# Kernel optimization log

Measured on AMD Instinct MI355X. Metric: run time of the kernel, lower is better.

Reference implementation:

```python
import jax, jax.numpy as jnp
import numpy as np

L_POS, L_DIR, H = 10, 4, 128
N = 1048576

def posenc(x, L):
    feats = [x]
    for j in range(L):
        s = (2.0 ** j) * x
        feats.append(jnp.sin(s))
        feats.append(jnp.cos(s))
    return jnp.concatenate(feats, axis=1)

def _w(key, fan_in, fan_out):
    return jax.random.normal(key, (fan_in, fan_out), dtype=jnp.float32) * (1.0 / np.sqrt(fan_in))

def setup_inputs() -> dict:
    key = jax.random.key(0)
    ks = jax.random.split(key, 16)
    pos = jax.random.normal(ks[0], (N, 3), dtype=jnp.float32)
    dirs = jax.random.normal(ks[1], (N, 3), dtype=jnp.float32)
    d_pos = 3 + 2 * 3 * L_POS  # 63
    d_dir = 3 + 2 * 3 * L_DIR  # 27
    inp = {
        'pos': pos, 'dirs': dirs,
        # block1: 4 hidden layers, ReLU everywhere incl. output (bias-free tcnn MLP)
        'b1_w0': _w(ks[2], d_pos, H), 'b1_w1': _w(ks[3], H, H),
        'b1_w2': _w(ks[4], H, H),    'b1_w3': _w(ks[5], H, H),
        'b1_w4': _w(ks[6], H, H),
        # block2: 3 hidden layers, linear output of width H+1
        'b2_w0': _w(ks[7], H + d_pos, H), 'b2_w1': _w(ks[8], H, H),
        'b2_w2': _w(ks[9], H, H),         'b2_w3': _w(ks[10], H, H + 1),
        # block3: 1 hidden layer of H//2, sigmoid output of width 3
        'b3_w0': _w(ks[11], H + d_dir, H // 2), 'b3_w1': _w(ks[12], H // 2, 3),
    }
    return inp

def reference(pos, dirs, b1_w0, b1_w1, b1_w2, b1_w3, b1_w4,
              b2_w0, b2_w1, b2_w2, b2_w3, b3_w0, b3_w1):
    relu = jax.nn.relu
    x_emb = posenc(pos, L_POS)   # [N, 63]
    d_emb = posenc(dirs, L_DIR)  # [N, 27]
    # block1: ReLU hidden + ReLU output
    h = relu(x_emb @ b1_w0)
    h = relu(h @ b1_w1)
    h = relu(h @ b1_w2)
    h = relu(h @ b1_w3)
    h = relu(h @ b1_w4)          # [N, 128]
    # block2: ReLU hidden, linear output
    g = relu(jnp.concatenate([h, x_emb], axis=1) @ b2_w0)
    g = relu(g @ b2_w1)
    g = relu(g @ b2_w2)
    g = g @ b2_w3                # [N, 129]
    sigma = jax.nn.relu(g[:, -1])
    feat = g[:, :-1]             # [N, 128]
    # block3: ReLU hidden, sigmoid output
    c = relu(jnp.concatenate([feat, d_emb], axis=1) @ b3_w0)
    color = jax.nn.sigmoid(c @ b3_w1)  # [N, 3]
    return (color, sigma)
```

## Files before the change

### kernel.cpp

```cpp
#include <hip/hip_runtime.h>
#include <hip/hip_bf16.h>

#define NTOT  1048576
#define MWG   128
#define BLK   256
#define ROWB  400
#define ACT_BYTES  (MWG * ROWB)

typedef __attribute__((ext_vector_type(8))) short  bf16x8;
typedef __attribute__((ext_vector_type(4))) float  f32x4;

__device__ __forceinline__ unsigned short f2bf(float f) {
  unsigned u = __float_as_uint(f);
  u += 0x7fffu + ((u >> 16) & 1u);
  return (unsigned short)(u >> 16);
}

__device__ __forceinline__ unsigned pk2bf(float lo, float hi) {
  float2 t; t.x = lo; t.y = hi;
  __hip_bfloat162 b = __float22bfloat162_rn(t);
  return *(unsigned*)&b;
}

__global__ __launch_bounds__(256) void prepack_k(
    const float* __restrict__ s0, const float* __restrict__ s1,
    const float* __restrict__ s2, const float* __restrict__ s3,
    const float* __restrict__ s4, const float* __restrict__ s5,
    const float* __restrict__ s6, const float* __restrict__ s7,
    const float* __restrict__ s8, const float* __restrict__ s9,
    const float* __restrict__ s10, unsigned short* __restrict__ dst)
{
  const int nw_[11]  = {128,128,128,128,128,128,128,128,144, 64, 16};
  const int kw_[11]  = { 64,128,128,128,128,192,128,128,128,192, 64};
  const int nc_[11]  = {128,128,128,128,128,128,128,128,129, 64,  3};
  const int k1_[11]  = { 63,128,128,128,128, 63,128,128,128, 27, 64};
  const int o1_[11]  = {  0,  0,  0,  0,  0,128,  0,  0,  0,128,  0};
  const int k2_[11]  = {999,999,999,999,999, 64,999,999,999, 64,999};
  const int do_[11]  = {0,8192,24576,40960,57344,73728,98304,114688,131072,149504,161792};

  int c = blockIdx.x;
  const float* src =
    c==0?s0: c==1?s1: c==2?s2: c==3?s3: c==4?s4: c==5?s5:
    c==6?s6: c==7?s7: c==8?s8: c==9?s9: s10;
  int nw=nw_[c], kw=kw_[c], nc=nc_[c], k1=k1_[c], o1=o1_[c], k2=k2_[c];
  int KS = kw >> 5;
  int total = nw * kw;
  for (int idx = blockIdx.y * blockDim.x + threadIdx.x; idx < total;
       idx += gridDim.y * blockDim.x) {
    int e   = idx & 7;
    int l15 = (idx >> 3) & 15;
    int lg  = (idx >> 7) & 3;
    int r   = idx >> 9;
    int ks  = r % KS;
    int nt  = r / KS;
    int n = nt * 16 + l15;
    int k = ks * 32 + lg * 8 + e;
    float v = 0.f;
    if (n < nc) {
      if (k < k1)       v = src[(o1 + k) * nc + n];
      else if (k >= k2) v = src[(k - k2) * nc + n];
    }
    dst[do_[c] + idx] = f2bf(v);
  }
}

template<int I0, int L>
__device__ __forceinline__ void posenc_store(unsigned char* actb, int row,
                                             float p0, float p1, float p2)
{
#pragma unroll
  for (int q = 0; q < 4; q++) {
    float hv[8];
#pragma unroll
    for (int e = 0; e < 8; e++) {
      const int i = I0 + q * 8 + e;
      float v;
      if (i == 0) v = p0;
      else if (i == 1) v = p1;
      else if (i == 2) v = p2;
      else {
        const int idx = i - 3, j = idx / 6, t = idx % 6;
        if (j < L) {
          const float sc = (float)(1 << j);
          const float a  = (t % 3 == 0 ? p0 : (t % 3 == 1 ? p1 : p2)) * sc;
          v = (t < 3) ? __sinf(a) : __cosf(a);
        } else v = 0.f;
      }
      hv[e] = v;
    }
    uint4 pk;
    pk.x = pk2bf(hv[0], hv[1]);
    pk.y = pk2bf(hv[2], hv[3]);
    pk.z = pk2bf(hv[4], hv[5]);
    pk.w = pk2bf(hv[6], hv[7]);
    *(uint4*)(actb + row * ROWB + (I0 + q * 8) * 2) = pk;
  }
}

template<int KS, int KB, int DST, bool RELU, bool MIDBAR, bool SIG>
__device__ __forceinline__ void layer22(
    unsigned char* actb, const unsigned short* __restrict__ wchunk,
    const unsigned* rbase, const unsigned* wbase,
    int lane, int wid, float* __restrict__ out, long grow0)
{
  const int l15 = lane & 15;
  const int lg  = lane >> 4;
  const int wn  = wid & 1;
  const unsigned short* wl = wchunk + (wn * 4) * (KS * 512) + lane * 8;
  const f32x4 vzero = {0.f, 0.f, 0.f, 0.f};
  f32x4 acc[4][4];

  {
    bf16x8 afr[4];
#pragma unroll
    for (int nt = 0; nt < 4; nt++)
      afr[nt] = *(const bf16x8*)(wl + (nt * KS) * 512);
    bf16x8 bfr4[4];
#pragma unroll
    for (int mq = 0; mq < 4; mq++)
      bfr4[mq] = *(const bf16x8*)(actb + rbase[mq] + KB * 2);
#pragma unroll
    for (int nt = 0; nt < 4; nt++)
#pragma unroll
      for (int mq = 0; mq < 4; mq++)
        acc[mq][nt] = __builtin_amdgcn_mfma_f32_16x16x32_bf16(
            afr[nt], bfr4[mq], vzero, 0, 0, 0);
  }
#pragma unroll
  for (int ks = 1; ks < KS; ks++) {
    bf16x8 afr[4];
#pragma unroll
    for (int nt = 0; nt < 4; nt++)
      afr[nt] = *(const bf16x8*)(wl + (nt * KS + ks) * 512);
    bf16x8 bfr4[4];
#pragma unroll
    for (int mq = 0; mq < 4; mq++)
      bfr4[mq] = *(const bf16x8*)(actb + rbase[mq] + (KB * 2 + ks * 64));
#pragma unroll
    for (int nt = 0; nt < 4; nt++)
#pragma unroll
      for (int mq = 0; mq < 4; mq++)
        acc[mq][nt] = __builtin_amdgcn_mfma_f32_16x16x32_bf16(
            afr[nt], bfr4[mq], acc[mq][nt], 0, 0, 0);
  }

  f32x4 accs[2];
  if (SIG) {
    unsigned sbase0 = ((2 * wid + 0) * 16 + l15) * ROWB + lg * 16;
    unsigned sbase1 = ((2 * wid + 1) * 16 + l15) * ROWB + lg * 16;
    {
      bf16x8 afs = *(const bf16x8*)(wchunk + (8 * KS) * 512 + lane * 8);
      bf16x8 b0 = *(const bf16x8*)(actb + sbase0 + KB * 2);
      bf16x8 b1 = *(const bf16x8*)(actb + sbase1 + KB * 2);
      accs[0] = __builtin_amdgcn_mfma_f32_16x16x32_bf16(afs, b0, vzero, 0, 0, 0);
      accs[1] = __builtin_amdgcn_mfma_f32_16x16x32_bf16(afs, b1, vzero, 0, 0, 0);
    }
#pragma unroll
    for (int ks = 1; ks < KS; ks++) {
      bf16x8 afs = *(const bf16x8*)(wchunk + (8 * KS + ks) * 512 + lane * 8);
      bf16x8 b0 = *(const bf16x8*)(actb + sbase0 + (KB * 2 + ks * 64));
      bf16x8 b1 = *(const bf16x8*)(actb + sbase1 + (KB * 2 + ks * 64));
      accs[0] = __builtin_amdgcn_mfma_f32_16x16x32_bf16(afs, b0, accs[0], 0, 0, 0);
      accs[1] = __builtin_amdgcn_mfma_f32_16x16x32_bf16(afs, b1, accs[1], 0, 0, 0);
    }
  }

  if (MIDBAR) __syncthreads();

#pragma unroll
  for (int mq = 0; mq < 4; mq++) {
#pragma unroll
    for (int nt = 0; nt < 4; nt++) {
      f32x4 v = acc[mq][nt];
      if (RELU) {
        v.x = fmaxf(v.x, 0.f); v.y = fmaxf(v.y, 0.f);
        v.z = fmaxf(v.z, 0.f); v.w = fmaxf(v.w, 0.f);
      }
      uint2 pk;
      pk.x = pk2bf(v.x, v.y);
      pk.y = pk2bf(v.z, v.w);
      *(uint2*)(actb + wbase[mq] + (DST * 2 + nt * 32)) = pk;
    }
  }
  if (SIG && lg == 0) {
#pragma unroll
    for (int j = 0; j < 2; j++) {
      int m = (2 * wid + j) * 16 + l15;
      out[3L * NTOT + grow0 + m] = fmaxf(accs[j].x, 0.f);
    }
  }
  __syncthreads();
}

__device__ __forceinline__ void layer_b3w0(
    unsigned char* actb, const unsigned short* __restrict__ wchunk,
    int lane, int wid)
{
  const int l15 = lane & 15;
  const int lg  = lane >> 4;
  const unsigned short* wl = wchunk + wid * (6 * 512) + lane * 8;
  const f32x4 vzero = {0.f, 0.f, 0.f, 0.f};
  f32x4 acc[8];

  unsigned rb[8];
#pragma unroll
  for (int mt = 0; mt < 8; mt++)
    rb[mt] = (mt * 16 + l15) * ROWB + lg * 16;

  {
    bf16x8 afr = *(const bf16x8*)(wl);
#pragma unroll
    for (int mt = 0; mt < 8; mt++) {
      bf16x8 b = *(const bf16x8*)(actb + rb[mt]);
      acc[mt] = __builtin_amdgcn_mfma_f32_16x16x32_bf16(afr, b, vzero, 0, 0, 0);
    }
  }
#pragma unroll
  for (int ks = 1; ks < 6; ks++) {
    bf16x8 afr = *(const bf16x8*)(wl + ks * 512);
#pragma unroll
    for (int half = 0; half < 2; half++) {
      bf16x8 bfr4[4];
#pragma unroll
      for (int mq = 0; mq < 4; mq++)
        bfr4[mq] = *(const bf16x8*)(actb + rb[half * 4 + mq] + ks * 64);
#pragma unroll
      for (int mq = 0; mq < 4; mq++)
        acc[half * 4 + mq] = __builtin_amdgcn_mfma_f32_16x16x32_bf16(
            afr, bfr4[mq], acc[half * 4 + mq], 0, 0, 0);
    }
  }

  __syncthreads();

#pragma unroll
  for (int mt = 0; mt < 8; mt++) {
    f32x4 v = acc[mt];
    v.x = fmaxf(v.x, 0.f); v.y = fmaxf(v.y, 0.f);
    v.z = fmaxf(v.z, 0.f); v.w = fmaxf(v.w, 0.f);
    uint2 pk;
    pk.x = pk2bf(v.x, v.y);
    pk.y = pk2bf(v.z, v.w);
    *(uint2*)(actb + (mt * 16 + l15) * ROWB + wid * 32 + lg * 8) = pk;
  }
  __syncthreads();
}

__device__ __forceinline__ void color_n(
    unsigned char* actb, const unsigned short* __restrict__ wchunk,
    int lane, int wid, float* __restrict__ out, long grow0)
{
  const int l15 = lane & 15;
  const int lg  = lane >> 4;
  const f32x4 vzero = {0.f, 0.f, 0.f, 0.f};
  f32x4 acc[2];
  unsigned cb0 = ((2 * wid + 0) * 16 + l15) * ROWB + lg * 16;
  unsigned cb1 = ((2 * wid + 1) * 16 + l15) * ROWB + lg * 16;
  {
    bf16x8 afr = *(const bf16x8*)(wchunk + lane * 8);
    bf16x8 b0 = *(const bf16x8*)(actb + cb0);
    bf16x8 b1 = *(const bf16x8*)(actb + cb1);
    acc[0] = __builtin_amdgcn_mfma_f32_16x16x32_bf16(afr, b0, vzero, 0, 0, 0);
    acc[1] = __builtin_amdgcn_mfma_f32_16x16x32_bf16(afr, b1, vzero, 0, 0, 0);
  }
  {
    bf16x8 afr = *(const bf16x8*)(wchunk + 512 + lane * 8);
    bf16x8 b0 = *(const bf16x8*)(actb + cb0 + 64);
    bf16x8 b1 = *(const bf16x8*)(actb + cb1 + 64);
    acc[0] = __builtin_amdgcn_mfma_f32_16x16x32_bf16(afr, b0, acc[0], 0, 0, 0);
    acc[1] = __builtin_amdgcn_mfma_f32_16x16x32_bf16(afr, b1, acc[1], 0, 0, 0);
  }
  if (lg == 0) {
#pragma unroll
    for (int j = 0; j < 2; j++) {
      int m = (2 * wid + j) * 16 + l15;
      long g3 = (grow0 + m) * 3;
      out[g3 + 0] = 1.f / (1.f + __expf(-acc[j].x));
      out[g3 + 1] = 1.f / (1.f + __expf(-acc[j].y));
      out[g3 + 2] = 1.f / (1.f + __expf(-acc[j].z));
    }
  }
}

__global__ __launch_bounds__(BLK, 2) void nerf_fused(
    const float* __restrict__ pos, const float* __restrict__ dirs,
    const unsigned short* __restrict__ wp, float* __restrict__ out)
{
  __shared__ unsigned char actb[ACT_BYTES];

  const int tid   = threadIdx.x;
  const int lane  = tid & 63;
  const int wid   = tid >> 6;
  const int wm    = wid >> 1;
  const int wn    = wid & 1;
  const long grow0 = (long)blockIdx.x * MWG;

  const int l15 = lane & 15;
  const int lg  = lane >> 4;

  unsigned rbase[4], wbase[4];
#pragma unroll
  for (int mq = 0; mq < 4; mq++) {
    int m = wm * 64 + mq * 16 + l15;
    rbase[mq] = m * ROWB + lg * 16;
    wbase[mq] = m * ROWB + wn * 128 + lg * 8;
  }

  const int row = wid * 32 + (lane & 31);
  const long g  = grow0 + row;

  {
    float p0 = pos[g * 3 + 0], p1 = pos[g * 3 + 1], p2 = pos[g * 3 + 2];
    if (lane < 32) posenc_store<0, 10>(actb, row, p0, p1, p2);
    else           posenc_store<32, 10>(actb, row, p0, p1, p2);
  }
  __syncthreads();

  layer22<2, 0, 64, true, false, false>(actb, wp +      0, rbase, wbase, lane, wid, out, grow0);
  layer22<4, 64, 64, true, true, false>(actb, wp +   8192, rbase, wbase, lane, wid, out, grow0);
  layer22<4, 64, 64, true, true, false>(actb, wp +  24576, rbase, wbase, lane, wid, out, grow0);
  layer22<4, 64, 64, true, true, false>(actb, wp +  40960, rbase, wbase, lane, wid, out, grow0);
  layer22<4, 64, 64, true, true, false>(actb, wp +  57344, rbase, wbase, lane, wid, out, grow0);
  layer22<6, 0, 64, true, true, false>(actb, wp +  73728, rbase, wbase, lane, wid, out, grow0);

  {
    float p0 = dirs[g * 3 + 0], p1 = dirs[g * 3 + 1], p2 = dirs[g * 3 + 2];
    if (lane < 32) posenc_store<0, 4>(actb, row, p0, p1, p2);
    else           posenc_store<32, 4>(actb, row, p0, p1, p2);
  }

  layer22<4, 64, 64, true, true, false>(actb, wp +  98304, rbase, wbase, lane, wid, out, grow0);
  layer22<4, 64, 64, true, true, false>(actb, wp + 114688, rbase, wbase, lane, wid, out, grow0);
  layer22<4, 64, 64, false, true, true>(actb, wp + 131072, rbase, wbase, lane, wid, out, grow0);
  layer_b3w0(actb, wp + 149504, lane, wid);
  color_n(actb, wp + 161792, lane, wid, out, grow0);
}

extern "C" void kernel_launch(void* const* d_in, const int* in_sizes, int n_in,
                              void* d_out, int out_size, void* d_ws, size_t ws_size,
                              hipStream_t stream)
{
  const float* pos  = (const float*)d_in[0];
  const float* dirs = (const float*)d_in[1];
  unsigned short* wpack = (unsigned short*)d_ws;
  float* out = (float*)d_out;

  prepack_k<<<dim3(11, 12, 1), 256, 0, stream>>>(
      (const float*)d_in[2], (const float*)d_in[3], (const float*)d_in[4],
      (const float*)d_in[5], (const float*)d_in[6], (const float*)d_in[7],
      (const float*)d_in[8], (const float*)d_in[9], (const float*)d_in[10],
      (const float*)d_in[11], (const float*)d_in[12], wpack);

  nerf_fused<<<NTOT / MWG, BLK, 0, stream>>>(pos, dirs, wpack, out);
}
```

Measured before the change: 331.2 us.

## Halve workgroup to 64 rows with two waves and use lightweight LDS barriers

Shrinks each workgroup from 128 rows and four waves to 64 rows and two waves. Each wave now covers all rows for its half of the output columns, and the b3 first layer is remapped so each wave computes two N-tiles. Full __syncthreads are replaced by an inline s_waitcnt lgkmcnt(0) plus s_barrier that does not wait on outstanding global memory operations. The goal is cheaper, finer-grained synchronization and more independent blocks per CU. The cost is less weight reuse per block and a dependence on the barrier only needing LDS ordering.

```diff
diff --git a/kernel.cpp b/kernel.cpp
--- a/kernel.cpp
+++ b/kernel.cpp
@@ -2,13 +2,17 @@
 #include <hip/hip_bf16.h>
 
 #define NTOT  1048576
-#define MWG   128
-#define BLK   256
+#define MWG   64
+#define BLK   128
 #define ROWB  400
 #define ACT_BYTES  (MWG * ROWB)
 
 typedef __attribute__((ext_vector_type(8))) short  bf16x8;
 typedef __attribute__((ext_vector_type(4))) float  f32x4;
+
+__device__ __forceinline__ void barL() {
+  asm volatile("s_waitcnt lgkmcnt(0)\n\ts_barrier" ::: "memory");
+}
 
 __device__ __forceinline__ unsigned short f2bf(float f) {
   unsigned u = __float_as_uint(f);
@@ -165,7 +169,7 @@
     }
   }
 
-  if (MIDBAR) __syncthreads();
+  if (MIDBAR) barL();
 
 #pragma unroll
   for (int mq = 0; mq < 4; mq++) {
@@ -189,7 +193,7 @@
       out[3L * NTOT + grow0 + m] = fmaxf(accs[j].x, 0.f);
     }
   }
-  __syncthreads();
+  barL();
 }
 
 __device__ __forceinline__ void layer_b3w0(
@@ -198,52 +202,54 @@
 {
   const int l15 = lane & 15;
   const int lg  = lane >> 4;
-  const unsigned short* wl = wchunk + wid * (6 * 512) + lane * 8;
+  const unsigned short* wl = wchunk + (2 * wid) * (6 * 512) + lane * 8;
   const f32x4 vzero = {0.f, 0.f, 0.f, 0.f};
-  f32x4 acc[8];
-
-  unsigned rb[8];
-#pragma unroll
-  for (int mt = 0; mt < 8; mt++)
+  f32x4 acc[4][2];
+
+  unsigned rb[4];
+#pragma unroll
+  for (int mt = 0; mt < 4; mt++)
     rb[mt] = (mt * 16 + l15) * ROWB + lg * 16;
 
   {
-    bf16x8 afr = *(const bf16x8*)(wl);
-#pragma unroll
-    for (int mt = 0; mt < 8; mt++) {
+    bf16x8 a0 = *(const bf16x8*)(wl);
+    bf16x8 a1 = *(const bf16x8*)(wl + 6 * 512);
+#pragma unroll
+    for (int mt = 0; mt < 4; mt++) {
       bf16x8 b = *(const bf16x8*)(actb + rb[mt]);
-      acc[mt] = __builtin_amdgcn_mfma_f32_16x16x32_bf16(afr, b, vzero, 0, 0, 0);
+      acc[mt][0] = __builtin_amdgcn_mfma_f32_16x16x32_bf16(a0, b, vzero, 0, 0, 0);
+      acc[mt][1] = __builtin_amdgcn_mfma_f32_16x16x32_bf16(a1, b, vzero, 0, 0, 0);
     }
   }
 #pragma unroll
   for (int ks = 1; ks < 6; ks++) {
-    bf16x8 afr = *(const bf16x8*)(wl + ks * 512);
-#pragma unroll
-    for (int half = 0; half < 2; half++) {
-      bf16x8 bfr4[4];
-#pragma unroll
-      for (int mq = 0; mq < 4; mq++)
-        bfr4[mq] = *(const bf16x8*)(actb + rb[half * 4 + mq] + ks * 64);
-#pragma unroll
-      for (int mq = 0; mq < 4; mq++)
-        acc[half * 4 + mq] = __builtin_amdgcn_mfma_f32_16x16x32_bf16(
-            afr, bfr4[mq], acc[half * 4 + mq], 0, 0, 0);
-    }
-  }
-
-  __syncthreads();
-
-#pragma unroll
-  for (int mt = 0; mt < 8; mt++) {
-    f32x4 v = acc[mt];
-    v.x = fmaxf(v.x, 0.f); v.y = fmaxf(v.y, 0.f);
-    v.z = fmaxf(v.z, 0.f); v.w = fmaxf(v.w, 0.f);
-    uint2 pk;
-    pk.x = pk2bf(v.x, v.y);
-    pk.y = pk2bf(v.z, v.w);
-    *(uint2*)(actb + (mt * 16 + l15) * ROWB + wid * 32 + lg * 8) = pk;
-  }
-  __syncthreads();
+    bf16x8 a0 = *(const bf16x8*)(wl + ks * 512);
+    bf16x8 a1 = *(const bf16x8*)(wl + (6 + ks) * 512);
+#pragma unroll
+    for (int mt = 0; mt < 4; mt++) {
+      bf16x8 b = *(const bf16x8*)(actb + rb[mt] + ks * 64);
+      acc[mt][0] = __builtin_amdgcn_mfma_f32_16x16x32_bf16(a0, b, acc[mt][0], 0, 0, 0);
+      acc[mt][1] = __builtin_amdgcn_mfma_f32_16x16x32_bf16(a1, b, acc[mt][1], 0, 0, 0);
+    }
+  }
+
+  barL();
+
+#pragma unroll
+  for (int mt = 0; mt < 4; mt++) {
+#pragma unroll
+    for (int n2 = 0; n2 < 2; n2++) {
+      f32x4 v = acc[mt][n2];
+      v.x = fmaxf(v.x, 0.f); v.y = fmaxf(v.y, 0.f);
+      v.z = fmaxf(v.z, 0.f); v.w = fmaxf(v.w, 0.f);
+      uint2 pk;
+      pk.x = pk2bf(v.x, v.y);
+      pk.y = pk2bf(v.z, v.w);
+      int col = (2 * wid + n2) * 16 + lg * 4;
+      *(uint2*)(actb + (mt * 16 + l15) * ROWB + col * 2) = pk;
+    }
+  }
+  barL();
 }
 
 __device__ __forceinline__ void color_n(
@@ -291,8 +297,6 @@
   const int tid   = threadIdx.x;
   const int lane  = tid & 63;
   const int wid   = tid >> 6;
-  const int wm    = wid >> 1;
-  const int wn    = wid & 1;
   const long grow0 = (long)blockIdx.x * MWG;
 
   const int l15 = lane & 15;
@@ -301,9 +305,9 @@
   unsigned rbase[4], wbase[4];
 #pragma unroll
   for (int mq = 0; mq < 4; mq++) {
-    int m = wm * 64 + mq * 16 + l15;
+    int m = mq * 16 + l15;
     rbase[mq] = m * ROWB + lg * 16;
-    wbase[mq] = m * ROWB + wn * 128 + lg * 8;
+    wbase[mq] = m * ROWB + wid * 128 + lg * 8;
   }
 
   const int row = wid * 32 + (lane & 31);
@@ -314,7 +318,7 @@
     if (lane < 32) posenc_store<0, 10>(actb, row, p0, p1, p2);
     else           posenc_store<32, 10>(actb, row, p0, p1, p2);
   }
-  __syncthreads();
+  barL();
 
   layer22<2, 0, 64, true, false, false>(actb, wp +      0, rbase, wbase, lane, wid, out, grow0);
   layer22<4, 64, 64, true, true, false>(actb, wp +   8192, rbase, wbase, lane, wid, out, grow0);
```

Result: slower. 339.6 us (+2.5%).

## Swizzle LDS activation rows with XOR and use lightweight LDS-only barriers

Applied to the files above, without the earlier changes.

Changes the LDS activation row stride from 400 to 384 bytes and applies an XOR swizzle of (row&7)<<4 to every read and write address, including positional encoding stores. The goal is to avoid LDS bank conflicts while keeping 16-byte alignment and using less shared memory. Read and write base addresses are precomputed per k-step parity and per n-tile. __syncthreads is replaced by an inline-asm lgkmcnt wait plus s_barrier, which does not wait on outstanding global memory operations. The address math adds some VALU work and is error-prone: every access must apply the same swizzle.

```diff
diff --git a/kernel.cpp b/kernel.cpp
--- a/kernel.cpp
+++ b/kernel.cpp
@@ -4,11 +4,15 @@
 #define NTOT  1048576
 #define MWG   128
 #define BLK   256
-#define ROWB  400
+#define ROWB  384
 #define ACT_BYTES  (MWG * ROWB)
 
 typedef __attribute__((ext_vector_type(8))) short  bf16x8;
 typedef __attribute__((ext_vector_type(4))) float  f32x4;
+
+__device__ __forceinline__ void barL() {
+  asm volatile("s_waitcnt lgkmcnt(0)\n\ts_barrier" ::: "memory");
+}
 
 __device__ __forceinline__ unsigned short f2bf(float f) {
   unsigned u = __float_as_uint(f);
@@ -93,14 +97,15 @@
     pk.y = pk2bf(hv[2], hv[3]);
     pk.z = pk2bf(hv[4], hv[5]);
     pk.w = pk2bf(hv[6], hv[7]);
-    *(uint4*)(actb + row * ROWB + (I0 + q * 8) * 2) = pk;
+    int b = (row * ROWB + (I0 + q * 8) * 2) ^ ((row & 7) << 4);
+    *(uint4*)(actb + b) = pk;
   }
 }
 
 template<int KS, int KB, int DST, bool RELU, bool MIDBAR, bool SIG>
 __device__ __forceinline__ void layer22(
     unsigned char* actb, const unsigned short* __restrict__ wchunk,
-    const unsigned* rbase, const unsigned* wbase,
+    const unsigned (*rb2)[2], const unsigned (*wb2)[4],
     int lane, int wid, float* __restrict__ out, long grow0)
 {
   const int l15 = lane & 15;
@@ -118,7 +123,7 @@
     bf16x8 bfr4[4];
 #pragma unroll
     for (int mq = 0; mq < 4; mq++)
-      bfr4[mq] = *(const bf16x8*)(actb + rbase[mq] + KB * 2);
+      bfr4[mq] = *(const bf16x8*)(actb + rb2[mq][0] + KB * 2);
 #pragma unroll
     for (int nt = 0; nt < 4; nt++)
 #pragma unroll
@@ -135,7 +140,7 @@
     bf16x8 bfr4[4];
 #pragma unroll
     for (int mq = 0; mq < 4; mq++)
-      bfr4[mq] = *(const bf16x8*)(actb + rbase[mq] + (KB * 2 + ks * 64));
+      bfr4[mq] = *(const bf16x8*)(actb + rb2[mq][ks & 1] + (KB * 2 + (ks >> 1) * 128));
 #pragma unroll
     for (int nt = 0; nt < 4; nt++)
 #pragma unroll
@@ -146,26 +151,21 @@
 
   f32x4 accs[2];
   if (SIG) {
-    unsigned sbase0 = ((2 * wid + 0) * 16 + l15) * ROWB + lg * 16;
-    unsigned sbase1 = ((2 * wid + 1) * 16 + l15) * ROWB + lg * 16;
-    {
-      bf16x8 afs = *(const bf16x8*)(wchunk + (8 * KS) * 512 + lane * 8);
-      bf16x8 b0 = *(const bf16x8*)(actb + sbase0 + KB * 2);
-      bf16x8 b1 = *(const bf16x8*)(actb + sbase1 + KB * 2);
-      accs[0] = __builtin_amdgcn_mfma_f32_16x16x32_bf16(afs, b0, vzero, 0, 0, 0);
-      accs[1] = __builtin_amdgcn_mfma_f32_16x16x32_bf16(afs, b1, vzero, 0, 0, 0);
-    }
-#pragma unroll
-    for (int ks = 1; ks < KS; ks++) {
+    accs[0] = vzero; accs[1] = vzero;
+#pragma unroll
+    for (int ks = 0; ks < KS; ks++) {
       bf16x8 afs = *(const bf16x8*)(wchunk + (8 * KS + ks) * 512 + lane * 8);
-      bf16x8 b0 = *(const bf16x8*)(actb + sbase0 + (KB * 2 + ks * 64));
-      bf16x8 b1 = *(const bf16x8*)(actb + sbase1 + (KB * 2 + ks * 64));
-      accs[0] = __builtin_amdgcn_mfma_f32_16x16x32_bf16(afs, b0, accs[0], 0, 0, 0);
-      accs[1] = __builtin_amdgcn_mfma_f32_16x16x32_bf16(afs, b1, accs[1], 0, 0, 0);
-    }
-  }
-
-  if (MIDBAR) __syncthreads();
+#pragma unroll
+      for (int j = 0; j < 2; j++) {
+        int m = (2 * wid + j) * 16 + l15;
+        int byt = (m * ROWB + KB * 2 + ks * 64 + lg * 16) ^ ((m & 7) << 4);
+        bf16x8 bfs = *(const bf16x8*)(actb + byt);
+        accs[j] = __builtin_amdgcn_mfma_f32_16x16x32_bf16(afs, bfs, accs[j], 0, 0, 0);
+      }
+    }
+  }
+
+  if (MIDBAR) barL();
 
 #pragma unroll
   for (int mq = 0; mq < 4; mq++) {
@@ -179,7 +179,7 @@
       uint2 pk;
       pk.x = pk2bf(v.x, v.y);
       pk.y = pk2bf(v.z, v.w);
-      *(uint2*)(actb + wbase[mq] + (DST * 2 + nt * 32)) = pk;
+      *(uint2*)(actb + wb2[mq][nt] + DST * 2) = pk;
     }
   }
   if (SIG && lg == 0) {
@@ -189,7 +189,7 @@
       out[3L * NTOT + grow0 + m] = fmaxf(accs[j].x, 0.f);
     }
   }
-  __syncthreads();
+  barL();
 }
 
 __device__ __forceinline__ void layer_b3w0(
@@ -202,16 +202,13 @@
   const f32x4 vzero = {0.f, 0.f, 0.f, 0.f};
   f32x4 acc[8];
 
-  unsigned rb[8];
-#pragma unroll
-  for (int mt = 0; mt < 8; mt++)
-    rb[mt] = (mt * 16 + l15) * ROWB + lg * 16;
-
   {
     bf16x8 afr = *(const bf16x8*)(wl);
 #pragma unroll
     for (int mt = 0; mt < 8; mt++) {
-      bf16x8 b = *(const bf16x8*)(actb + rb[mt]);
+      int m = mt * 16 + l15;
+      int byt = (m * ROWB + lg * 16) ^ ((m & 7) << 4);
+      bf16x8 b = *(const bf16x8*)(actb + byt);
       acc[mt] = __builtin_amdgcn_mfma_f32_16x16x32_bf16(afr, b, vzero, 0, 0, 0);
     }
   }
@@ -219,19 +216,15 @@
   for (int ks = 1; ks < 6; ks++) {
     bf16x8 afr = *(const bf16x8*)(wl + ks * 512);
 #pragma unroll
-    for (int half = 0; half < 2; half++) {
-      bf16x8 bfr4[4];
-#pragma unroll
-      for (int mq = 0; mq < 4; mq++)
-        bfr4[mq] = *(const bf16x8*)(actb + rb[half * 4 + mq] + ks * 64);
-#pragma unroll
-      for (int mq = 0; mq < 4; mq++)
-        acc[half * 4 + mq] = __builtin_amdgcn_mfma_f32_16x16x32_bf16(
-            afr, bfr4[mq], acc[half * 4 + mq], 0, 0, 0);
-    }
-  }
-
-  __syncthreads();
+    for (int mt = 0; mt < 8; mt++) {
+      int m = mt * 16 + l15;
+      int byt = (m * ROWB + ks * 64 + lg * 16) ^ ((m & 7) << 4);
+      bf16x8 b = *(const bf16x8*)(actb + byt);
+      acc[mt] = __builtin_amdgcn_mfma_f32_16x16x32_bf16(afr, b, acc[mt], 0, 0, 0);
+    }
+  }
+
+  barL();
 
 #pragma unroll
   for (int mt = 0; mt < 8; mt++) {
@@ -241,9 +234,11 @@
     uint2 pk;
     pk.x = pk2bf(v.x, v.y);
     pk.y = pk2bf(v.z, v.w);
-    *(uint2*)(actb + (mt * 16 + l15) * ROWB + wid * 32 + lg * 8) = pk;
-  }
-  __syncthreads();
+    int m = mt * 16 + l15;
+    int byt = (m * ROWB + wid * 32 + lg * 8) ^ ((m & 7) << 4);
+    *(uint2*)(actb + byt) = pk;
+  }
+  barL();
 }
 
 __device__ __forceinline__ void color_n(
@@ -254,21 +249,22 @@
   const int lg  = lane >> 4;
   const f32x4 vzero = {0.f, 0.f, 0.f, 0.f};
   f32x4 acc[2];
-  unsigned cb0 = ((2 * wid + 0) * 16 + l15) * ROWB + lg * 16;
-  unsigned cb1 = ((2 * wid + 1) * 16 + l15) * ROWB + lg * 16;
-  {
-    bf16x8 afr = *(const bf16x8*)(wchunk + lane * 8);
-    bf16x8 b0 = *(const bf16x8*)(actb + cb0);
-    bf16x8 b1 = *(const bf16x8*)(actb + cb1);
-    acc[0] = __builtin_amdgcn_mfma_f32_16x16x32_bf16(afr, b0, vzero, 0, 0, 0);
-    acc[1] = __builtin_amdgcn_mfma_f32_16x16x32_bf16(afr, b1, vzero, 0, 0, 0);
-  }
-  {
-    bf16x8 afr = *(const bf16x8*)(wchunk + 512 + lane * 8);
-    bf16x8 b0 = *(const bf16x8*)(actb + cb0 + 64);
-    bf16x8 b1 = *(const bf16x8*)(actb + cb1 + 64);
-    acc[0] = __builtin_amdgcn_mfma_f32_16x16x32_bf16(afr, b0, acc[0], 0, 0, 0);
-    acc[1] = __builtin_amdgcn_mfma_f32_16x16x32_bf16(afr, b1, acc[1], 0, 0, 0);
+  int m0 = (2 * wid + 0) * 16 + l15;
+  int m1 = (2 * wid + 1) * 16 + l15;
+#pragma unroll
+  for (int ks = 0; ks < 2; ks++) {
+    bf16x8 afr = *(const bf16x8*)(wchunk + ks * 512 + lane * 8);
+    int b0a = (m0 * ROWB + ks * 64 + lg * 16) ^ ((m0 & 7) << 4);
+    int b1a = (m1 * ROWB + ks * 64 + lg * 16) ^ ((m1 & 7) << 4);
+    bf16x8 b0 = *(const bf16x8*)(actb + b0a);
+    bf16x8 b1 = *(const bf16x8*)(actb + b1a);
+    if (ks == 0) {
+      acc[0] = __builtin_amdgcn_mfma_f32_16x16x32_bf16(afr, b0, vzero, 0, 0, 0);
+      acc[1] = __builtin_amdgcn_mfma_f32_16x16x32_bf16(afr, b1, vzero, 0, 0, 0);
+    } else {
+      acc[0] = __builtin_amdgcn_mfma_f32_16x16x32_bf16(afr, b0, acc[0], 0, 0, 0);
+      acc[1] = __builtin_amdgcn_mfma_f32_16x16x32_bf16(afr, b1, acc[1], 0, 0, 0);
+    }
   }
   if (lg == 0) {
 #pragma unroll
@@ -298,12 +294,17 @@
   const int l15 = lane & 15;
   const int lg  = lane >> 4;
 
-  unsigned rbase[4], wbase[4];
+  unsigned rb2[4][2], wb2[4][4];
 #pragma unroll
   for (int mq = 0; mq < 4; mq++) {
     int m = wm * 64 + mq * 16 + l15;
-    rbase[mq] = m * ROWB + lg * 16;
-    wbase[mq] = m * ROWB + wn * 128 + lg * 8;
+    unsigned sw = (unsigned)((m & 7) << 4);
+    unsigned base = (unsigned)(m * ROWB);
+    rb2[mq][0] = (base + lg * 16) ^ sw;
+    rb2[mq][1] = (base + 64 + lg * 16) ^ sw;
+#pragma unroll
+    for (int nt = 0; nt < 4; nt++)
+      wb2[mq][nt] = (base + wn * 128 + nt * 32 + lg * 8) ^ sw;
   }
 
   const int row = wid * 32 + (lane & 31);
@@ -314,14 +315,14 @@
     if (lane < 32) posenc_store<0, 10>(actb, row, p0, p1, p2);
     else           posenc_store<32, 10>(actb, row, p0, p1, p2);
   }
-  __syncthreads();
-
-  layer22<2, 0, 64, true, false, false>(actb, wp +      0, rbase, wbase, lane, wid, out, grow0);
-  layer22<4, 64, 64, true, true, false>(actb, wp +   8192, rbase, wbase, lane, wid, out, grow0);
-  layer22<4, 64, 64, true, true, false>(actb, wp +  24576, rbase, wbase, lane, wid, out, grow0);
-  layer22<4, 64, 64, true, true, false>(actb, wp +  40960, rbase, wbase, lane, wid, out, grow0);
-  layer22<4, 64, 64, true, true, false>(actb, wp +  57344, rbase, wbase, lane, wid, out, grow0);
-  layer22<6, 0, 64, true, true, false>(actb, wp +  73728, rbase, wbase, lane, wid, out, grow0);
+  barL();
+
+  layer22<2, 0, 64, true, false, false>(actb, wp +      0, rb2, wb2, lane, wid, out, grow0);
+  layer22<4, 64, 64, true, true, false>(actb, wp +   8192, rb2, wb2, lane, wid, out, grow0);
+  layer22<4, 64, 64, true, true, false>(actb, wp +  24576, rb2, wb2, lane, wid, out, grow0);
+  layer22<4, 64, 64, true, true, false>(actb, wp +  40960, rb2, wb2, lane, wid, out, grow0);
+  layer22<4, 64, 64, true, true, false>(actb, wp +  57344, rb2, wb2, lane, wid, out, grow0);
+  layer22<6, 0, 64, true, true, false>(actb, wp +  73728, rb2, wb2, lane, wid, out, grow0);
 
   {
     float p0 = dirs[g * 3 + 0], p1 = dirs[g * 3 + 1], p2 = dirs[g * 3 + 2];
@@ -329,9 +330,9 @@
     else           posenc_store<32, 4>(actb, row, p0, p1, p2);
   }
 
-  layer22<4, 64, 64, true, true, false>(actb, wp +  98304, rbase, wbase, lane, wid, out, grow0);
-  layer22<4, 64, 64, true, true, false>(actb, wp + 114688, rbase, wbase, lane, wid, out, grow0);
-  layer22<4, 64, 64, false, true, true>(actb, wp + 131072, rbase, wbase, lane, wid, out, grow0);
+  layer22<4, 64, 64, true, true, false>(actb, wp +  98304, rb2, wb2, lane, wid, out, grow0);
+  layer22<4, 64, 64, true, true, false>(actb, wp + 114688, rb2, wb2, lane, wid, out, grow0);
+  layer22<4, 64, 64, false, true, true>(actb, wp + 131072, rb2, wb2, lane, wid, out, grow0);
   layer_b3w0(actb, wp + 149504, lane, wid);
   color_n(actb, wp + 161792, lane, wid, out, grow0);
 }
```

New measurement: 328.2 us. No clear change (-0.9%).
